# Kernel tuning notes

Hardware: AMD Instinct MI355X
Metric: run time of the kernel (lower is better)

Reference implementation:

```python
import jax, jax.numpy as jnp
import numpy as np

N_U = 50000   # num user nodes
N_I = 50000   # num item nodes
D = 64        # in_size == out_size
H = 128       # SemanticAttention hidden size (default)
E = 500000    # edges per meta-path graph
NEG_SLOPE = 0.01


def setup_inputs() -> dict:
    key = jax.random.key(0)
    ks = jax.random.split(key, 24)
    rn = lambda k, shp, s=0.1: jax.random.normal(k, shp, jnp.float32) * s
    ri = lambda k, shp, n: jax.random.randint(k, shp, 0, n, dtype=jnp.int32)
    return dict(
        feat_user=rn(ks[0], (N_U, D)), feat_item=rn(ks[1], (N_I, D)),
        attn_l=rn(ks[2], (4, D)), attn_r=rn(ks[3], (4, D)),
        W_gc=rn(ks[4], (4, D, D)), b_gc=jnp.zeros((4, D), jnp.float32),
        sa_rel_W1=rn(ks[5], (D, H)), sa_rel_b1=jnp.zeros((H,), jnp.float32), sa_rel_w2=rn(ks[6], (H,)),
        sa_u_W1=rn(ks[7], (D, H)), sa_u_b1=jnp.zeros((H,), jnp.float32), sa_u_w2=rn(ks[8], (H,)),
        sa_i_W1=rn(ks[9], (D, H)), sa_i_b1=jnp.zeros((H,), jnp.float32), sa_i_w2=rn(ks[10], (H,)),
        rel_u_src=ri(ks[11], (2, E), N_I), rel_u_dst=ri(ks[12], (2, E), N_U),
        rel_i_src=ri(ks[13], (2, E), N_U), rel_i_dst=ri(ks[14], (2, E), N_I),
        mp_u_src=ri(ks[15], (2, E), N_U), mp_u_dst=ri(ks[16], (2, E), N_U),
        mp_i_src=ri(ks[17], (2, E), N_I), mp_i_dst=ri(ks[18], (2, E), N_I),
    )


def _edge_softmax(e, dst, n_dst):
    # segment-wise (per destination node) softmax over irregular edges
    m = jax.ops.segment_max(e, dst, num_segments=n_dst)
    ex = jnp.exp(e - m[dst])
    s = jax.ops.segment_sum(ex, dst, num_segments=n_dst)
    return ex / s[dst]


def _heco_gat(src, dst, feat_src, feat_dst, al, ar, n_dst):
    # HeCoGATConv: el = sum(ft_src*attn_l), er = sum(ft_dst*attn_r)
    el = feat_src @ al  # (N_src,)
    er = feat_dst @ ar  # (N_dst,)
    e = jax.nn.leaky_relu(el[src] + er[dst], NEG_SLOPE)  # (E,)
    a = _edge_softmax(e, dst, n_dst)
    out = jax.ops.segment_sum(feat_src[src] * a[:, None], dst, num_segments=n_dst)
    return jax.nn.elu(out)


def _graph_conv(src, dst, feat, W, b, n):
    # DGL GraphConv with norm='both', activation=elu
    ones = jnp.ones(src.shape, jnp.float32)
    deg_out = jax.ops.segment_sum(ones, src, num_segments=n)
    deg_in = jax.ops.segment_sum(ones, dst, num_segments=n)
    no = jnp.where(deg_out > 0, deg_out, 1.0) ** -0.5
    ni = jnp.where(deg_in > 0, deg_in, 1.0) ** -0.5
    h = feat * no[:, None]
    agg = jax.ops.segment_sum(h[src], dst, num_segments=n)
    agg = agg * ni[:, None]
    return jax.nn.elu(agg @ W + b)


def _semantic_attention(z, W1, b1, w2):
    # z: (N, M, D) -> (N, D)
    w = (jnp.tanh(z @ W1 + b1) @ w2).mean(0)  # (M,)
    beta = jax.nn.softmax(w)
    return jnp.einsum('nmd,m->nd', z, beta)


def reference(feat_user, feat_item, attn_l, attn_r, W_gc, b_gc,
              sa_rel_W1, sa_rel_b1, sa_rel_w2,
              sa_u_W1, sa_u_b1, sa_u_w2,
              sa_i_W1, sa_i_b1, sa_i_w2,
              rel_u_src, rel_u_dst, rel_i_src, rel_i_dst,
              mp_u_src, mp_u_dst, mp_i_src, mp_i_dst):
    # --- RelationalAGG: HeCo GAT over schema-level relations ---
    zu = jnp.stack([
        _heco_gat(rel_u_src[0], rel_u_dst[0], feat_item, feat_user, attn_l[0], attn_r[0], N_U),
        _heco_gat(rel_u_src[1], rel_u_dst[1], feat_item, feat_user, attn_l[1], attn_r[1], N_U),
    ], axis=1)  # (N_U, 2, D)
    rel_u = _semantic_attention(zu, sa_rel_W1, sa_rel_b1, sa_rel_w2)
    zi = jnp.stack([
        _heco_gat(rel_i_src[0], rel_i_dst[0], feat_user, feat_item, attn_l[2], attn_r[2], N_I),
        _heco_gat(rel_i_src[1], rel_i_dst[1], feat_user, feat_item, attn_l[3], attn_r[3], N_I),
    ], axis=1)
    rel_i = _semantic_attention(zi, sa_rel_W1, sa_rel_b1, sa_rel_w2)
    # --- HAN layers: GraphConv over meta-path reachable graphs ---
    hu = jnp.stack([
        _graph_conv(mp_u_src[0], mp_u_dst[0], feat_user, W_gc[0], b_gc[0], N_U),
        _graph_conv(mp_u_src[1], mp_u_dst[1], feat_user, W_gc[1], b_gc[1], N_U),
    ], axis=1)
    han_u = _semantic_attention(hu, sa_u_W1, sa_u_b1, sa_u_w2)
    hi = jnp.stack([
        _graph_conv(mp_i_src[0], mp_i_dst[0], feat_item, W_gc[2], b_gc[2], N_I),
        _graph_conv(mp_i_src[1], mp_i_dst[1], feat_item, W_gc[3], b_gc[3], N_I),
    ], axis=1)
    han_i = _semantic_attention(hi, sa_i_W1, sa_i_b1, sa_i_w2)
    user_emb = rel_u + han_u
    item_emb = rel_i + han_i
    return jnp.concatenate([user_emb, item_emb], axis=0)  # (N_U + N_I, D)
```

## Files before the change

### kernel.cpp

```cpp
#include <hip/hip_runtime.h>
#include <math.h>

#define NU 50000
#define NI 50000
#define NN 50000
#define DD 64
#define HHID 128
#define EE 500000
#define NEG_SLOPE 0.01f
#define NBKT 196
#define CAP 3072
#define TILE 8192
#define TPG 62
#define P1T 512
#define NIMG 12
#define P1B (NIMG * TPG)
#define AGGB 1563
#define SEMB 512

typedef _Float16 half_t;
typedef _Float16 half8 __attribute__((ext_vector_type(8)));
typedef float f32x4 __attribute__((ext_vector_type(4)));
union H4 { uint2 u; half_t h[4]; };
union H8 { uint4 u; half_t h[8]; };
union HS { half8 h; int i[4]; uint4 u; };
union HC { unsigned short us; half_t h; };

struct Ptr4c { const float* p[4]; };
struct Ptr4m { float*       p[4]; };
struct EdgeArgs { const int* src[8]; const int* dst[8]; };
struct GatArgs { const half_t* fsrc[4]; half_t* zout[4]; };
struct GcArgs  { const half_t* feat[4]; half_t* hout[4]; };
struct WArgs   { const float* el[4]; const float* er[4]; const int* deg_src; };
struct SemArgs { const half_t* z[4]; const float* W1[4]; const float* b1[4]; const float* w2[4]; };
struct PrepArgs {
    const float* featI; const float* featU;
    Ptr4c vi; Ptr4c vu; Ptr4m oi; Ptr4m ou;
    half_t* FBI; half_t* FBU;
    const float* W_gc; half_t* W16;
};

__global__ __launch_bounds__(P1T) void build_kernel(EdgeArgs a, int* __restrict__ ccnt,
                                                    int* __restrict__ coarse, PrepArgs pa) {
    __shared__ int bc_cnt[256], bc_scan[256], bc_start[256], bc_cur[256], bc_gbase[256];
    __shared__ int stage[TILE];
    int t = threadIdx.x;
    if (blockIdx.x >= P1B) {
        int pb = blockIdx.x - P1B;
        if (pb == 3125) {
            if (t < 256) {
                int g = t >> 6;
                int lane = t & 63;
                int cl = lane & 15, quad = lane >> 4;
#pragma unroll
                for (int nt = 0; nt < 4; nt++) {
#pragma unroll
                    for (int kh = 0; kh < 2; kh++) {
                        H8 o;
#pragma unroll
                        for (int j = 0; j < 8; j++) {
                            int k = kh * 32 + quad * 8 + j;
                            int n = nt * 16 + cl;
                            o.h[j] = (half_t)pa.W_gc[g * 4096 + k * 64 + n];
                        }
                        *(uint4*)(pa.W16 + ((g * 8 + nt * 2 + kh) * 64 + lane) * 8) = o.u;
                    }
                }
            }
            return;
        }
        int ob = pb * 2 + (t >> 8);
        int t256 = t & 255;
        const float* feat; Ptr4c vecs; Ptr4m outs; half_t* fb16; int bb;
        if (ob < 3125) { feat = pa.featI; vecs = pa.vi; outs = pa.oi; fb16 = pa.FBI; bb = ob; }
        else           { feat = pa.featU; vecs = pa.vu; outs = pa.ou; fb16 = pa.FBU; bb = ob - 3125; }
        int w = bb * 4 + (t256 >> 6);
        int lane = t256 & 63;
        int sub = lane >> 4, r = lane & 15;
        int node = w * 4 + sub;
        float4 f = *(const float4*)(feat + node * DD + r * 4);
        H4 o16;
        o16.h[0] = (half_t)f.x; o16.h[1] = (half_t)f.y; o16.h[2] = (half_t)f.z; o16.h[3] = (half_t)f.w;
        *(uint2*)(fb16 + node * DD + r * 4) = o16.u;
#pragma unroll
        for (int j = 0; j < 4; j++) {
            float4 vv = *(const float4*)(vecs.p[j] + r * 4);
            float val = f.x * vv.x + f.y * vv.y + f.z * vv.z + f.w * vv.w;
            val += __shfl_down(val, 8);
            val += __shfl_down(val, 4);
            val += __shfl_down(val, 2);
            val += __shfl_down(val, 1);
            if (r == 0) outs.p[j][node] = val;
        }
        return;
    }
    int g = blockIdx.x / TPG;
    int tile = blockIdx.x % TPG;
    int e0 = tile * TILE;
    int tile_n = min(TILE, EE - e0);
    bool cnt_only = g >= 8;
    const int* gk = (cnt_only ? a.src[g - 4] : a.dst[g]) + e0;
    const int* gs = cnt_only ? gk : (a.src[g] + e0);
    if (t < 256) bc_cnt[t] = 0;
    __syncthreads();
    for (int pos = t * 4; pos < tile_n; pos += P1T * 4) {
        int4 k4 = *(const int4*)(gk + pos);
        atomicAdd(&bc_cnt[k4.x >> 8], 1);
        atomicAdd(&bc_cnt[k4.y >> 8], 1);
        atomicAdd(&bc_cnt[k4.z >> 8], 1);
        atomicAdd(&bc_cnt[k4.w >> 8], 1);
    }
    __syncthreads();
    if (t < 256) bc_scan[t] = bc_cnt[t];
    __syncthreads();
    for (int off = 1; off < 256; off <<= 1) {
        int v = (t < 256 && t >= off) ? bc_scan[t - off] : 0;
        __syncthreads();
        if (t < 256) bc_scan[t] += v;
        __syncthreads();
    }
    if (t < 256) {
        int st = bc_scan[t] - bc_cnt[t];
        bc_start[t] = st;
        bc_cur[t] = st;
        bc_gbase[t] = (t < NBKT && bc_cnt[t] > 0) ? atomicAdd(&ccnt[g * NBKT + t], bc_cnt[t]) : 0;
    }
    __syncthreads();
    for (int pos = t * 4; pos < tile_n; pos += P1T * 4) {
        int4 k4 = *(const int4*)(gk + pos);
        int4 s4;
        if (cnt_only) { s4 = make_int4(0, 0, 0, 0); }
        else          { s4 = *(const int4*)(gs + pos); }
        int b0 = k4.x >> 8, b1 = k4.y >> 8, b2 = k4.z >> 8, b3 = k4.w >> 8;
        int sl0 = atomicAdd(&bc_cur[b0], 1);
        int sl1 = atomicAdd(&bc_cur[b1], 1);
        int sl2 = atomicAdd(&bc_cur[b2], 1);
        int sl3 = atomicAdd(&bc_cur[b3], 1);
        stage[sl0] = s4.x | ((k4.x & 255) << 16) | (b0 << 24);
        stage[sl1] = s4.y | ((k4.y & 255) << 16) | (b1 << 24);
        stage[sl2] = s4.z | ((k4.z & 255) << 16) | (b2 << 24);
        stage[sl3] = s4.w | ((k4.w & 255) << 16) | (b3 << 24);
    }
    __syncthreads();
    for (int j = t; j < tile_n; j += P1T) {
        int p = stage[j];
        int b = (unsigned)p >> 24;
        int pos = bc_gbase[b] + (j - bc_start[b]);
        if (pos < CAP) coarse[(g * NBKT + b) * CAP + pos] = p & 0x00FFFFFF;
    }
}

__global__ __launch_bounds__(256) void degcnt_kernel(const int* __restrict__ ccnt,
                                                     const int* __restrict__ coarse,
                                                     int* __restrict__ DEG_SRC) {
    __shared__ int cnt[256];
    int t = threadIdx.x;
    int g2 = blockIdx.x / NBKT;
    int b = blockIdx.x % NBKT;
    int img = 8 + g2;
    int n = min(ccnt[img * NBKT + b], CAP);
    cnt[t] = 0;
    __syncthreads();
    const int* pairs = coarse + (img * NBKT + b) * CAP;
    for (int i = t; i < n; i += 256) atomicAdd(&cnt[(pairs[i] >> 16) & 255], 1);
    __syncthreads();
    int v = (b << 8) + t;
    if (v < NN) DEG_SRC[g2 * NN + v] = cnt[t];
}

__global__ __launch_bounds__(256) void part2_kernel(const int* __restrict__ ccnt,
                                                    const int* __restrict__ coarse,
                                                    WArgs wa,
                                                    int* __restrict__ bucket,
                                                    int2* __restrict__ RD) {
    __shared__ int sb[256];
    __shared__ int cnt5[256], off5[256], s2[256];
    __shared__ int ordered[CAP];
    int t = threadIdx.x;
    int g = blockIdx.x / NBKT;
    int b = blockIdx.x % NBKT;
    int ccv = (t < NBKT) ? min(ccnt[g * NBKT + t], CAP) : 0;
    sb[t] = ccv;
    cnt5[t] = 0;
    __syncthreads();
    for (int off = 1; off < 256; off <<= 1) {
        int vv = (t >= off) ? sb[t - off] : 0;
        __syncthreads();
        sb[t] += vv;
        __syncthreads();
    }
    int base = (b > 0) ? sb[b - 1] : 0;
    int n = sb[b] - base;
    int node0 = b << 8;
    const int* pairs = coarse + (g * NBKT + b) * CAP;
    for (int i = t; i < n; i += 256) atomicAdd(&cnt5[pairs[i] >> 16], 1);
    __syncthreads();
    int myc = cnt5[t];
    s2[t] = myc;
    __syncthreads();
    for (int off = 1; off < 256; off <<= 1) {
        int vv = (t >= off) ? s2[t - off] : 0;
        __syncthreads();
        s2[t] += vv;
        __syncthreads();
    }
    int ex = s2[t] - myc;
    off5[t] = ex;
    int v = node0 + t;
    if (v < NN) RD[g * NN + v] = make_int2(base + ex, myc);
    __syncthreads();
    int nm1 = n - 1;
    for (int ib = t; ib < n; ib += 1024) {
        int p[4];
#pragma unroll
        for (int u = 0; u < 4; u++) {
            int i = ib + u * 256;
            p[u] = pairs[(i < n) ? i : nm1];
        }
        float w[4];
        if (g < 4) {
            float a0[4], a1[4];
#pragma unroll
            for (int u = 0; u < 4; u++) a0[u] = wa.el[g][p[u] & 0xFFFF];
#pragma unroll
            for (int u = 0; u < 4; u++) a1[u] = wa.er[g][node0 + (p[u] >> 16)];
#pragma unroll
            for (int u = 0; u < 4; u++) {
                float e = a0[u] + a1[u];
                e = (e >= 0.f) ? e : NEG_SLOPE * e;
                w[u] = __expf(e);
            }
        } else {
            int dv[4];
#pragma unroll
            for (int u = 0; u < 4; u++) dv[u] = wa.deg_src[(g - 4) * NN + (p[u] & 0xFFFF)];
#pragma unroll
            for (int u = 0; u < 4; u++) w[u] = __builtin_amdgcn_rsqf((float)dv[u]);
        }
#pragma unroll
        for (int u = 0; u < 4; u++) {
            int i = ib + u * 256;
            if (i < n) {
                HC cv; cv.h = (half_t)w[u];
                int slot = atomicAdd(&off5[p[u] >> 16], 1);
                ordered[slot] = (p[u] & 0xFFFF) | ((int)cv.us << 16);
            }
        }
    }
    __syncthreads();
    int* bko = bucket + g * EE + base;
    for (int i = t; i < n; i += 256) bko[i] = ordered[i];
}

__global__ __launch_bounds__(256) void agg_kernel(GatArgs ga, GcArgs gc,
                                                  const half_t* __restrict__ W16,
                                                  const float* __restrict__ b_gc,
                                                  const int2* __restrict__ RD,
                                                  const int* __restrict__ bucket) {
    __shared__ half_t AS[32][64];
    int g = blockIdx.x / AGGB;
    int nb = blockIdx.x % AGGB;
    int t = threadIdx.x;
    int wv = t >> 6, lane = t & 63;
    int q = lane >> 3, r = lane & 7;
    int v = nb * 32 + wv * 8 + q;
    bool vok = v < NN;
    int2 rd = RD[g * NN + (vok ? v : 0)];
    int start = rd.x;
    int dg = vok ? rd.y : 0;
    const int* bk = bucket + g * EE;
    const half_t* feat = (g < 4) ? ga.fsrc[g] : gc.feat[g - 4];
    int roff = r << 3;
    int obase = lane & 56;
    HS acc[4];
#pragma unroll
    for (int a = 0; a < 4; a++)
#pragma unroll
        for (int j = 0; j < 4; j++) acc[a].i[j] = 0;
    float s_l = 0.f;
    for (int b8 = 0; b8 < dg; b8 += 8) {
        int rem = dg - b8;
        int p = bk[start + b8 + ((r < rem) ? r : 0)];
#pragma unroll
        for (int j = 0; j < 8; j++) {
            if (j < rem) {
                int pj = __shfl(p, obase + j);
                HC wj; wj.us = (unsigned short)((unsigned)pj >> 16);
                s_l += (float)wj.h;
                HS row; row.u = *(const uint4*)(feat + (((pj & 0xFFFF) << 6) + roff));
                half_t wh = wj.h;
                half8 ws = {wh, wh, wh, wh, wh, wh, wh, wh};
                acc[j & 3].h += row.h * ws;
            }
        }
    }
    acc[0].h += acc[1].h;
    acc[2].h += acc[3].h;
    acc[0].h += acc[2].h;
    if (g < 4) {
        float inv = (dg > 0) ? __builtin_amdgcn_rcpf(s_l) : 0.f;
        H8 o;
#pragma unroll
        for (int i = 0; i < 8; i++) {
            float x = (float)acc[0].h[i] * inv;
            x = (x > 0.f) ? x : (__expf(x) - 1.f);
            o.h[i] = (half_t)x;
        }
        if (vok) *(uint4*)(ga.zout[g] + (v << 7) + roff) = o.u;
        return;
    }
    int gg = g - 4;
    {
        float niv = (dg > 0) ? __builtin_amdgcn_rsqf((float)dg) : 1.0f;
        H8 o;
#pragma unroll
        for (int i = 0; i < 8; i++) o.h[i] = (half_t)((float)acc[0].h[i] * niv);
        *(uint4*)(&AS[wv * 8 + q][roff]) = o.u;
    }
    __syncthreads();
    int cl = lane & 15, quad = lane >> 4;
    int tl = wv >> 1;
    const half_t* ar = &AS[tl * 16 + cl][quad * 8];
    half8 A0 = *(const half8*)(ar);
    half8 A1 = *(const half8*)(ar + 32);
    const half_t* wbase = W16 + gg * 8 * 64 * 8;
    half_t* hout = gc.hout[gg];
#pragma unroll
    for (int u = 0; u < 2; u++) {
        int nt = (wv & 1) * 2 + u;
        float bb = b_gc[gg * 64 + nt * 16 + cl];
        f32x4 c = {bb, bb, bb, bb};
        half8 B0 = *(const half8*)(wbase + ((nt * 2 + 0) * 64 + lane) * 8);
        half8 B1 = *(const half8*)(wbase + ((nt * 2 + 1) * 64 + lane) * 8);
        c = __builtin_amdgcn_mfma_f32_16x16x32_f16(A0, B0, c, 0, 0, 0);
        c = __builtin_amdgcn_mfma_f32_16x16x32_f16(A1, B1, c, 0, 0, 0);
#pragma unroll
        for (int r_ = 0; r_ < 4; r_++) {
            int node = nb * 32 + tl * 16 + quad * 4 + r_;
            if (node < NN) {
                float x = c[r_];
                x = (x > 0.f) ? x : (__expf(x) - 1.f);
                hout[node * 128 + nt * 16 + cl] = (half_t)x;
            }
        }
    }
}

__global__ __launch_bounds__(256) void sem_att_kernel(SemArgs sa, float* __restrict__ wsum) {
    __shared__ half_t As[2][4][1024];
    __shared__ float s0[4], s1[4];
    int inst = blockIdx.x / SEMB;
    int blk  = blockIdx.x % SEMB;
    int t = threadIdx.x;
    int wv = t >> 6, lane = t & 63;
    int quad = lane >> 4, cl = lane & 15;
    const half_t* z = sa.z[inst];
    const float* W1 = sa.W1[inst];
    half8 Bf[2][2];
    float b1v[2], w2v[2];
#pragma unroll
    for (int u = 0; u < 2; u++) {
        int nt = wv * 2 + u;
        int n = nt * 16 + cl;
#pragma unroll
        for (int kh = 0; kh < 2; kh++) {
#pragma unroll
            for (int j = 0; j < 8; j++) {
                int k = kh * 32 + quad * 8 + j;
                Bf[u][kh][j] = (half_t)W1[k * HHID + n];
            }
        }
        b1v[u] = sa.b1[inst][nt * 16 + cl];
        w2v[u] = sa.w2[inst][nt * 16 + cl];
    }
    float local0 = 0.f, local1 = 0.f;
    int K = (6250 - blk + SEMB - 1) / SEMB;
    int B = (K + 3) / 4;

#define SEM_STAGE(buf, bb) { \
    int k_ = 4 * (bb) + wv; \
    if (k_ < K) { \
        int tp_ = blk + k_ * SEMB; \
        int m_ = (tp_ >= 3125) ? 1 : 0; \
        int tm_ = tp_ - m_ * 3125; \
        int n_ = lane >> 3; \
        int j_ = (lane & 7) * 8; \
        const half_t* sA_ = z + (size_t)(tm_ * 16 + n_) * 128 + m_ * 64 + j_; \
        const half_t* sB_ = z + (size_t)(tm_ * 16 + 8 + n_) * 128 + m_ * 64 + j_; \
        __builtin_amdgcn_global_load_lds( \
            (const __attribute__((address_space(1))) unsigned int*)sA_, \
            (__attribute__((address_space(3))) unsigned int*)(&As[buf][wv][0]), 16, 0, 0); \
        __builtin_amdgcn_global_load_lds( \
            (const __attribute__((address_space(1))) unsigned int*)sB_, \
            (__attribute__((address_space(3))) unsigned int*)(&As[buf][wv][512]), 16, 0, 0); \
    } }

    int cur = 0;
    SEM_STAGE(0, 0);
    for (int b = 0; b < B; b++) {
        if (b + 1 < B) {
            SEM_STAGE(cur ^ 1, b + 1);
            asm volatile("s_waitcnt vmcnt(2)" ::: "memory");
        } else {
            asm volatile("s_waitcnt vmcnt(0)" ::: "memory");
        }
        __builtin_amdgcn_sched_barrier(0);
        __builtin_amdgcn_s_barrier();
#pragma unroll
        for (int i = 0; i < 4; i++) {
            int k = 4 * b + i;
            if (k < K) {
                int tile = blk + k * SEMB;
                const half_t* ar = &As[cur][i][cl * 64 + quad * 8];
                half8 A0 = *(const half8*)(ar);
                half8 A1 = *(const half8*)(ar + 32);
                float sumv = 0.f;
#pragma unroll
                for (int u = 0; u < 2; u++) {
                    f32x4 c = {0.f, 0.f, 0.f, 0.f};
                    c = __builtin_amdgcn_mfma_f32_16x16x32_f16(A0, Bf[u][0], c, 0, 0, 0);
                    c = __builtin_amdgcn_mfma_f32_16x16x32_f16(A1, Bf[u][1], c, 0, 0, 0);
#pragma unroll
                    for (int r = 0; r < 4; r++) {
                        float xv = c[r] + b1v[u];
                        float ev = __expf(2.f * xv);
                        float th = 1.f - 2.f * __builtin_amdgcn_rcpf(ev + 1.f);
                        sumv += th * w2v[u];
                    }
                }
                if (tile < 3125) local0 += sumv; else local1 += sumv;
            }
        }
        __builtin_amdgcn_s_barrier();
        cur ^= 1;
    }
#undef SEM_STAGE
#pragma unroll
    for (int off = 32; off > 0; off >>= 1) {
        local0 += __shfl_down(local0, off);
        local1 += __shfl_down(local1, off);
    }
    if (lane == 0) { s0[wv] = local0; s1[wv] = local1; }
    __syncthreads();
    if (t == 0) {
        float a0 = s0[0] + s0[1] + s0[2] + s0[3];
        float a1 = s1[0] + s1[1] + s1[2] + s1[3];
        if (a0 != 0.f) atomicAdd(&wsum[inst * 2 + 0], a0);
        if (a1 != 0.f) atomicAdd(&wsum[inst * 2 + 1], a1);
    }
}

__global__ void combine_kernel(const half_t* __restrict__ ZU, const half_t* __restrict__ ZI,
                               const half_t* __restrict__ HU, const half_t* __restrict__ HI,
                               const float* __restrict__ wsum, float* __restrict__ out) {
    int gid = blockIdx.x * blockDim.x + threadIdx.x;
    if (gid >= (NU + NI) * 16) return;
    int node = gid >> 4;
    int c4 = (gid & 15) * 4;
    const half_t* zb; const half_t* hb;
    float wr0, wr1, wh0, wh1;
    int idx;
    if (node < NU) {
        zb = ZU; hb = HU; idx = node;
        wr0 = wsum[0]; wr1 = wsum[1]; wh0 = wsum[4]; wh1 = wsum[5];
    } else {
        zb = ZI; hb = HI; idx = node - NU;
        wr0 = wsum[2]; wr1 = wsum[3]; wh0 = wsum[6]; wh1 = wsum[7];
    }
    const float inv_n = 1.0f / 50000.0f;
    wr0 *= inv_n; wr1 *= inv_n; wh0 *= inv_n; wh1 *= inv_n;
    float m = fmaxf(wr0, wr1);
    float e0 = __expf(wr0 - m), e1 = __expf(wr1 - m);
    float br0 = e0 / (e0 + e1), br1 = e1 / (e0 + e1);
    m = fmaxf(wh0, wh1);
    e0 = __expf(wh0 - m); e1 = __expf(wh1 - m);
    float bh0 = e0 / (e0 + e1), bh1 = e1 / (e0 + e1);
    H4 z0, z1, h0, h1;
    z0.u = *(const uint2*)(zb + idx * 128 + c4);
    z1.u = *(const uint2*)(zb + idx * 128 + 64 + c4);
    h0.u = *(const uint2*)(hb + idx * 128 + c4);
    h1.u = *(const uint2*)(hb + idx * 128 + 64 + c4);
    float4 o;
    o.x = (float)z0.h[0] * br0 + (float)z1.h[0] * br1 + (float)h0.h[0] * bh0 + (float)h1.h[0] * bh1;
    o.y = (float)z0.h[1] * br0 + (float)z1.h[1] * br1 + (float)h0.h[1] * bh0 + (float)h1.h[1] * bh1;
    o.z = (float)z0.h[2] * br0 + (float)z1.h[2] * br1 + (float)h0.h[2] * bh0 + (float)h1.h[2] * bh1;
    o.w = (float)z0.h[3] * br0 + (float)z1.h[3] * br1 + (float)h0.h[3] * bh0 + (float)h1.h[3] * bh1;
    *(float4*)(out + node * 64 + c4) = o;
}

extern "C" void kernel_launch(void* const* d_in, const int* in_sizes, int n_in,
                              void* d_out, int out_size, void* d_ws, size_t ws_size,
                              hipStream_t stream) {
    const float* feat_user = (const float*)d_in[0];
    const float* feat_item = (const float*)d_in[1];
    const float* attn_l    = (const float*)d_in[2];
    const float* attn_r    = (const float*)d_in[3];
    const float* W_gc      = (const float*)d_in[4];
    const float* b_gc      = (const float*)d_in[5];
    const float* sa_rel_W1 = (const float*)d_in[6];
    const float* sa_rel_b1 = (const float*)d_in[7];
    const float* sa_rel_w2 = (const float*)d_in[8];
    const float* sa_u_W1   = (const float*)d_in[9];
    const float* sa_u_b1   = (const float*)d_in[10];
    const float* sa_u_w2   = (const float*)d_in[11];
    const float* sa_i_W1   = (const float*)d_in[12];
    const float* sa_i_b1   = (const float*)d_in[13];
    const float* sa_i_w2   = (const float*)d_in[14];
    const int* rel_u_src = (const int*)d_in[15];
    const int* rel_u_dst = (const int*)d_in[16];
    const int* rel_i_src = (const int*)d_in[17];
    const int* rel_i_dst = (const int*)d_in[18];
    const int* mp_u_src  = (const int*)d_in[19];
    const int* mp_u_dst  = (const int*)d_in[20];
    const int* mp_i_src  = (const int*)d_in[21];
    const int* mp_i_dst  = (const int*)d_in[22];

    half_t* ZU   = (half_t*)d_ws;
    half_t* ZI   = ZU + NN * 128;
    half_t* HU   = ZI + NN * 128;
    half_t* HI   = HU + NN * 128;
    half_t* FBU  = HI + NN * 128;
    half_t* FBI  = FBU + NN * 64;
    float*  DI   = (float*)(FBI + NN * 64);
    float*  DU   = DI + 4 * NN;
    int2*   RD   = (int2*)(DU + 4 * NN);
    int*    BUCKET = (int*)(RD + 8 * NN);
    int*    CCNT = BUCKET + 8 * EE;
    int*    DEG_SRC = CCNT + 12 * 256;
    float*  WSUM = (float*)(DEG_SRC + 4 * NN);
    half_t* W16  = (half_t*)(WSUM + 8);
    int*    COARSE = (int*)d_ws;

    hipMemsetAsync(CCNT, 0, (size_t)(12 * 256 + 4 * NN) * sizeof(int) + 8 * sizeof(float), stream);

    PrepArgs pa;
    pa.featI = feat_item; pa.featU = feat_user;
    pa.vi = Ptr4c{{ attn_l + 0 * DD, attn_l + 1 * DD, attn_r + 2 * DD, attn_r + 3 * DD }};
    pa.oi = Ptr4m{{ DI, DI + NI, DI + 2 * NI, DI + 3 * NI }};
    pa.vu = Ptr4c{{ attn_l + 2 * DD, attn_l + 3 * DD, attn_r + 0 * DD, attn_r + 1 * DD }};
    pa.ou = Ptr4m{{ DU, DU + NU, DU + 2 * NU, DU + 3 * NU }};
    pa.FBI = FBI; pa.FBU = FBU;
    pa.W_gc = W_gc; pa.W16 = W16;

    EdgeArgs ea;
    ea.src[0] = rel_u_src;      ea.dst[0] = rel_u_dst;
    ea.src[1] = rel_u_src + EE; ea.dst[1] = rel_u_dst + EE;
    ea.src[2] = rel_i_src;      ea.dst[2] = rel_i_dst;
    ea.src[3] = rel_i_src + EE; ea.dst[3] = rel_i_dst + EE;
    ea.src[4] = mp_u_src;       ea.dst[4] = mp_u_dst;
    ea.src[5] = mp_u_src + EE;  ea.dst[5] = mp_u_dst + EE;
    ea.src[6] = mp_i_src;       ea.dst[6] = mp_i_dst;
    ea.src[7] = mp_i_src + EE;  ea.dst[7] = mp_i_dst + EE;

    build_kernel<<<P1B + 3126, P1T, 0, stream>>>(ea, CCNT, COARSE, pa);
    degcnt_kernel<<<4 * NBKT, 256, 0, stream>>>(CCNT, COARSE, DEG_SRC);

    WArgs wa;
    wa.el[0] = DI;      wa.er[0] = DU + 2 * NU;
    wa.el[1] = DI + NI; wa.er[1] = DU + 3 * NU;
    wa.el[2] = DU;      wa.er[2] = DI + 2 * NI;
    wa.el[3] = DU + NU; wa.er[3] = DI + 3 * NI;
    wa.deg_src = DEG_SRC;
    part2_kernel<<<8 * NBKT, 256, 0, stream>>>(CCNT, COARSE, wa, BUCKET, RD);

    GatArgs ga;
    ga.fsrc[0] = FBI; ga.zout[0] = ZU;
    ga.fsrc[1] = FBI; ga.zout[1] = ZU + 64;
    ga.fsrc[2] = FBU; ga.zout[2] = ZI;
    ga.fsrc[3] = FBU; ga.zout[3] = ZI + 64;
    GcArgs gc;
    gc.feat[0] = FBU; gc.hout[0] = HU;
    gc.feat[1] = FBU; gc.hout[1] = HU + 64;
    gc.feat[2] = FBI; gc.hout[2] = HI;
    gc.feat[3] = FBI; gc.hout[3] = HI + 64;
    agg_kernel<<<8 * AGGB, 256, 0, stream>>>(ga, gc, W16, b_gc, RD, BUCKET);

    SemArgs sa;
    sa.z[0] = ZU; sa.W1[0] = sa_rel_W1; sa.b1[0] = sa_rel_b1; sa.w2[0] = sa_rel_w2;
    sa.z[1] = ZI; sa.W1[1] = sa_rel_W1; sa.b1[1] = sa_rel_b1; sa.w2[1] = sa_rel_w2;
    sa.z[2] = HU; sa.W1[2] = sa_u_W1;   sa.b1[2] = sa_u_b1;   sa.w2[2] = sa_u_w2;
    sa.z[3] = HI; sa.W1[3] = sa_i_W1;   sa.b1[3] = sa_i_b1;   sa.w2[3] = sa_i_w2;
    sem_att_kernel<<<4 * SEMB, 256, 0, stream>>>(sa, WSUM);

    combine_kernel<<<((NU + NI) * 16 + 255) / 256, 256, 0, stream>>>(ZU, ZI, HU, HI, WSUM, (float*)d_out);
}
```

Baseline: 320.6 us.

## Fold degree counting into part2 and compute GraphConv norm weights in aggregation

Removes the separate degcnt kernel launch by giving part2 four extra block groups that count source degrees. Because those degrees may not be ready while part2 runs, the GraphConv rsqrt(deg_out) edge weights are no longer computed in part2. They are computed in agg_kernel from DEG_SRC as each batch of edge indices is loaded. The shared tile AS is also padded from 64 to 72 columns, likely to avoid LDS bank conflicts. The cost is an extra gather from the degree table inside the aggregation loop for the GraphConv graphs.

```diff
diff --git a/kernel.cpp b/kernel.cpp
--- a/kernel.cpp
+++ b/kernel.cpp
@@ -31,7 +31,7 @@
 struct EdgeArgs { const int* src[8]; const int* dst[8]; };
 struct GatArgs { const half_t* fsrc[4]; half_t* zout[4]; };
 struct GcArgs  { const half_t* feat[4]; half_t* hout[4]; };
-struct WArgs   { const float* el[4]; const float* er[4]; const int* deg_src; };
+struct WArgs   { const float* el[4]; const float* er[4]; };
 struct SemArgs { const half_t* z[4]; const float* W1[4]; const float* b1[4]; const float* w2[4]; };
 struct PrepArgs {
     const float* featI; const float* featU;
@@ -150,35 +150,29 @@
     }
 }
 
-__global__ __launch_bounds__(256) void degcnt_kernel(const int* __restrict__ ccnt,
-                                                     const int* __restrict__ coarse,
-                                                     int* __restrict__ DEG_SRC) {
-    __shared__ int cnt[256];
-    int t = threadIdx.x;
-    int g2 = blockIdx.x / NBKT;
-    int b = blockIdx.x % NBKT;
-    int img = 8 + g2;
-    int n = min(ccnt[img * NBKT + b], CAP);
-    cnt[t] = 0;
-    __syncthreads();
-    const int* pairs = coarse + (img * NBKT + b) * CAP;
-    for (int i = t; i < n; i += 256) atomicAdd(&cnt[(pairs[i] >> 16) & 255], 1);
-    __syncthreads();
-    int v = (b << 8) + t;
-    if (v < NN) DEG_SRC[g2 * NN + v] = cnt[t];
-}
-
 __global__ __launch_bounds__(256) void part2_kernel(const int* __restrict__ ccnt,
                                                     const int* __restrict__ coarse,
                                                     WArgs wa,
                                                     int* __restrict__ bucket,
-                                                    int2* __restrict__ RD) {
+                                                    int2* __restrict__ RD,
+                                                    int* __restrict__ DEG_SRC) {
     __shared__ int sb[256];
     __shared__ int cnt5[256], off5[256], s2[256];
     __shared__ int ordered[CAP];
     int t = threadIdx.x;
     int g = blockIdx.x / NBKT;
     int b = blockIdx.x % NBKT;
+    if (g >= 8) {
+        int n = min(ccnt[g * NBKT + b], CAP);
+        cnt5[t] = 0;
+        __syncthreads();
+        const int* pairs = coarse + (g * NBKT + b) * CAP;
+        for (int i = t; i < n; i += 256) atomicAdd(&cnt5[(pairs[i] >> 16) & 255], 1);
+        __syncthreads();
+        int v = (b << 8) + t;
+        if (v < NN) DEG_SRC[(g - 8) * NN + v] = cnt5[t];
+        return;
+    }
     int ccv = (t < NBKT) ? min(ccnt[g * NBKT + t], CAP) : 0;
     sb[t] = ccv;
     cnt5[t] = 0;
@@ -230,20 +224,16 @@
                 e = (e >= 0.f) ? e : NEG_SLOPE * e;
                 w[u] = __expf(e);
             }
-        } else {
-            int dv[4];
-#pragma unroll
-            for (int u = 0; u < 4; u++) dv[u] = wa.deg_src[(g - 4) * NN + (p[u] & 0xFFFF)];
-#pragma unroll
-            for (int u = 0; u < 4; u++) w[u] = __builtin_amdgcn_rsqf((float)dv[u]);
         }
 #pragma unroll
         for (int u = 0; u < 4; u++) {
             int i = ib + u * 256;
             if (i < n) {
-                HC cv; cv.h = (half_t)w[u];
+                int ent;
+                if (g < 4) { HC cv; cv.h = (half_t)w[u]; ent = (p[u] & 0xFFFF) | ((int)cv.us << 16); }
+                else       { ent = p[u] & 0xFFFF; }
                 int slot = atomicAdd(&off5[p[u] >> 16], 1);
-                ordered[slot] = (p[u] & 0xFFFF) | ((int)cv.us << 16);
+                ordered[slot] = ent;
             }
         }
     }
@@ -256,8 +246,9 @@
                                                   const half_t* __restrict__ W16,
                                                   const float* __restrict__ b_gc,
                                                   const int2* __restrict__ RD,
-                                                  const int* __restrict__ bucket) {
-    __shared__ half_t AS[32][64];
+                                                  const int* __restrict__ bucket,
+                                                  const int* __restrict__ DEG_SRC) {
+    __shared__ half_t AS[32][72];
     int g = blockIdx.x / AGGB;
     int nb = blockIdx.x % AGGB;
     int t = threadIdx.x;
@@ -270,6 +261,7 @@
     int dg = vok ? rd.y : 0;
     const int* bk = bucket + g * EE;
     const half_t* feat = (g < 4) ? ga.fsrc[g] : gc.feat[g - 4];
+    const int* degtab = DEG_SRC + (g >= 4 ? (g - 4) * NN : 0);
     int roff = r << 3;
     int obase = lane & 56;
     HS acc[4];
@@ -281,6 +273,11 @@
     for (int b8 = 0; b8 < dg; b8 += 8) {
         int rem = dg - b8;
         int p = bk[start + b8 + ((r < rem) ? r : 0)];
+        if (g >= 4) {
+            int dsv = degtab[p & 0xFFFF];
+            HC cv; cv.h = (half_t)__builtin_amdgcn_rsqf((float)dsv);
+            p = (p & 0xFFFF) | ((int)cv.us << 16);
+        }
 #pragma unroll
         for (int j = 0; j < 8; j++) {
             if (j < rem) {
@@ -553,15 +550,13 @@
     ea.src[7] = mp_i_src + EE;  ea.dst[7] = mp_i_dst + EE;
 
     build_kernel<<<P1B + 3126, P1T, 0, stream>>>(ea, CCNT, COARSE, pa);
-    degcnt_kernel<<<4 * NBKT, 256, 0, stream>>>(CCNT, COARSE, DEG_SRC);
 
     WArgs wa;
     wa.el[0] = DI;      wa.er[0] = DU + 2 * NU;
     wa.el[1] = DI + NI; wa.er[1] = DU + 3 * NU;
     wa.el[2] = DU;      wa.er[2] = DI + 2 * NI;
     wa.el[3] = DU + NU; wa.er[3] = DI + 3 * NI;
-    wa.deg_src = DEG_SRC;
-    part2_kernel<<<8 * NBKT, 256, 0, stream>>>(CCNT, COARSE, wa, BUCKET, RD);
+    part2_kernel<<<12 * NBKT, 256, 0, stream>>>(CCNT, COARSE, wa, BUCKET, RD, DEG_SRC);
 
     GatArgs ga;
     ga.fsrc[0] = FBI; ga.zout[0] = ZU;
@@ -573,7 +568,7 @@
     gc.feat[1] = FBU; gc.hout[1] = HU + 64;
     gc.feat[2] = FBI; gc.hout[2] = HI;
     gc.feat[3] = FBI; gc.hout[3] = HI + 64;
-    agg_kernel<<<8 * AGGB, 256, 0, stream>>>(ga, gc, W16, b_gc, RD, BUCKET);
+    agg_kernel<<<8 * AGGB, 256, 0, stream>>>(ga, gc, W16, b_gc, RD, BUCKET, DEG_SRC);
 
     SemArgs sa;
     sa.z[0] = ZU; sa.W1[0] = sa_rel_W1; sa.b1[0] = sa_rel_b1; sa.w2[0] = sa_rel_w2;
```

Measured after the change: 312.6 us. -2.5%, faster.
